# Optimization experiments

Measured on AMD Instinct MI355X. Metric: run time of the kernel, lower is better.

## Reference

```python
import jax, jax.numpy as jnp
import numpy as np

N = 50000
E = 400000
IN_C = 512
HID = 64
OUT_C = 40
H = 4
NEG_SLOPE = 0.2
EPS = 1e-16  # PyG softmax denominator epsilon


def glorot(key, shape, fan_in, fan_out):
    limit = float(np.sqrt(6.0 / (fan_in + fan_out)))
    return jax.random.uniform(key, shape, jnp.float32, -limit, limit)


def setup_inputs() -> dict:
    key = jax.random.key(0)
    ks = jax.random.split(key, 8)
    x = jax.random.normal(ks[0], (N, IN_C), jnp.float32)
    # random edges guaranteed to have src != dst (forward adds exactly one self-loop per node)
    src = jax.random.randint(ks[1], (E,), 0, N)
    off = jax.random.randint(ks[2], (E,), 1, N)
    dst = (src + off) % N
    edge_index = jnp.stack([src, dst], axis=0).astype(jnp.int64)
    W1 = glorot(ks[3], (IN_C, H * HID), IN_C, H * HID)
    b1 = jnp.zeros((H * HID,), jnp.float32)
    W2 = glorot(ks[4], (H * HID, H * OUT_C), H * HID, H * OUT_C)
    b2 = jnp.zeros((OUT_C,), jnp.float32)
    return {"x": x, "edge_index": edge_index, "W1": W1, "b1": b1, "W2": W2, "b2": b2}


def _supergat_layer(x, src, dst, W, b, heads, out_c, concat):
    n = x.shape[0]
    h = (x @ W).reshape(n, heads, out_c)            # [N,H,C]
    x_i = h[dst]                                    # [E',H,C] target
    x_j = h[src]                                    # [E',H,C] source
    # MX attention with return_logits=True inside message(): plain dot-product logits
    alpha = jnp.sum(x_i * x_j, axis=-1)             # [E',H]
    alpha = jax.nn.leaky_relu(alpha, NEG_SLOPE)
    # segment softmax over destination node
    amax = jax.ops.segment_max(alpha, dst, num_segments=n)
    alpha = jnp.exp(alpha - amax[dst])
    denom = jax.ops.segment_sum(alpha, dst, num_segments=n)
    alpha = alpha / (denom[dst] + EPS)
    out = jax.ops.segment_sum(x_j * alpha[:, :, None], dst, num_segments=n)  # [N,H,C]
    if concat:
        out = out.reshape(n, heads * out_c)
    else:
        out = out.mean(axis=1)
    return out + b


def reference(x, edge_index, W1, b1, W2, b2):
    # add_self_loops (input edges contain no self loops by construction)
    loop = jnp.arange(N, dtype=edge_index.dtype)
    src = jnp.concatenate([edge_index[0], loop])
    dst = jnp.concatenate([edge_index[1], loop])
    h = _supergat_layer(x, src, dst, W1, b1, H, HID, concat=True)
    h = jax.nn.elu(h)
    out = _supergat_layer(h, src, dst, W2, b2, H, OUT_C, concat=False)
    logp = jax.nn.log_softmax(out, axis=-1)
    att_loss = jnp.zeros((1,), jnp.float32)  # eval mode: get_attention_loss returns 0
    return logp, att_loss
```

## Files before the change

### kernel.cpp

```cpp
#include <hip/hip_runtime.h>
#include <cstddef>
#include <cstdint>

#define HEADS 4
#define OUTC  40
#define NEG   0.2f
#define EPSV  1e-16f

typedef __bf16 bf16x8 __attribute__((ext_vector_type(8)));
typedef float  floatx4 __attribute__((ext_vector_type(4)));

__device__ __forceinline__ void split_bf16(float a, unsigned& hi, unsigned& lo) {
  unsigned u = __float_as_uint(a);
  hi = u >> 16;
  float hf = __uint_as_float(u & 0xFFFF0000u);
  lo = __float_as_uint(a - hf) >> 16;
}

__device__ __forceinline__ void dma16(const void* g, void* l) {
  __builtin_amdgcn_global_load_lds(
      (const __attribute__((address_space(1))) unsigned int*)g,
      (__attribute__((address_space(3))) unsigned int*)l, 16, 0, 0);
}

__global__ void hist_k(const int* __restrict__ dst, int* __restrict__ cnt, int E) {
  int e = blockIdx.x * blockDim.x + threadIdx.x;
  if (e < E) atomicAdd(&cnt[dst[e]], 1);
}

__global__ __launch_bounds__(1024) void scanA_k(const int* __restrict__ cnt,
                                                int* __restrict__ rp,
                                                int* __restrict__ bsum, int n) {
  __shared__ int sh[1024];
  int i = blockIdx.x * 1024 + threadIdx.x;
  int v = (i < n) ? cnt[i] : 0;
  sh[threadIdx.x] = v;
  __syncthreads();
  for (int d = 1; d < 1024; d <<= 1) {
    int t = (threadIdx.x >= d) ? sh[threadIdx.x - d] : 0;
    __syncthreads();
    sh[threadIdx.x] += t;
    __syncthreads();
  }
  if (i < n) rp[i] = sh[threadIdx.x] - v;
  if (threadIdx.x == 1023) bsum[blockIdx.x] = sh[1023];
}

__global__ void scanC_k(int* __restrict__ rp, const int* __restrict__ bsum,
                        int n, int nb) {
  int i = blockIdx.x * blockDim.x + threadIdx.x;
  if (i < n) {
    int b = i >> 10;
    int off = 0;
    for (int j = 0; j < b; ++j) off += bsum[j];
    rp[i] += off;
  }
  if (i == 0) {
    int tot = 0;
    for (int j = 0; j < nb; ++j) tot += bsum[j];
    rp[n] = tot;
  }
}

__global__ void scatter_k(const int* __restrict__ src, const int* __restrict__ dst,
                          const int* __restrict__ rp, int* __restrict__ cur,
                          int* __restrict__ out, int E) {
  int e = blockIdx.x * blockDim.x + threadIdx.x;
  if (e < E) {
    int d = dst[e];
    int p = rp[d] + atomicAdd(&cur[d], 1);
    out[p] = src[e];
  }
}

__global__ void convW_k(const float* __restrict__ W1, unsigned short* __restrict__ Wh1,
                        unsigned short* __restrict__ Wl1,
                        const float* __restrict__ W2, unsigned short* __restrict__ Wh2,
                        unsigned short* __restrict__ Wl2) {
  int id = blockIdx.x * 256 + threadIdx.x;
  if (id < 256 * 512) {
    int n = id >> 9, k = id & 511;
    unsigned h, l;
    split_bf16(W1[k * 256 + n], h, l);
    Wh1[id] = (unsigned short)h;
    Wl1[id] = (unsigned short)l;
  } else {
    int id2 = id - 256 * 512;
    int n = id2 >> 8, k = id2 & 255;
    int hh = n >> 6, c = n & 63;
    float a = (c < OUTC) ? W2[k * 160 + hh * OUTC + c] : 0.f;
    unsigned h, l;
    split_bf16(a, h, l);
    Wh2[id2] = (unsigned short)h;
    Wl2[id2] = (unsigned short)l;
  }
}

template <bool A_FP32, bool COMPACT>
__global__ __launch_bounds__(256) void gemm_dma(const void* Aptr_h, const void* Aptr_l,
                                                const unsigned short* __restrict__ Bh,
                                                const unsigned short* __restrict__ Bl,
                                                float* __restrict__ C, int M, int K) {
  __shared__ __align__(16) unsigned char lds[65536];
  const int tid = threadIdx.x;
  const int lane = tid & 63;
  const int w = tid >> 6;
  const int wr = w >> 1, wc = w & 1;
  const int row0 = blockIdx.y * 128;
  const int col0 = blockIdx.x * 128;
  const int fr = lane & 15, fq = lane >> 4;
  const int swz8 = fr & 7;
  const int swz4 = (fr & 3) ^ ((fr >> 2) & 1);
  const int srcA8 = (lane & 7) ^ (lane >> 3);
  const int srcB4 = (lane & 3) ^ ((lane >> 2) & 3) ^ ((lane >> 4) & 1);

  floatx4 acc[4][4];
#pragma unroll
  for (int i = 0; i < 4; ++i)
#pragma unroll
    for (int j = 0; j < 4; ++j) acc[i][j] = (floatx4){0.f, 0.f, 0.f, 0.f};

  const float* Af32 = (const float*)Aptr_h;
  const unsigned short* Agh = (const unsigned short*)Aptr_h;
  const unsigned short* Agl = (const unsigned short*)Aptr_l;

#define DMA_TILE(K0, BASE)                                                          \
  do {                                                                              \
    if (A_FP32) {                                                                   \
      _Pragma("unroll") for (int t = 0; t < 4; ++t) {                               \
        int arow = w * 32 + t * 8 + (lane >> 3);                                    \
        int gr = row0 + arow; gr = gr < M ? gr : M - 1;                             \
        dma16(&Af32[(size_t)gr * K + (K0) + srcA8 * 4],                             \
              lds + (BASE) + (size_t)(w * 32 + t * 8) * 128);                       \
      }                                                                             \
    } else {                                                                        \
      _Pragma("unroll") for (int t = 0; t < 2; ++t) {                               \
        int arow = w * 32 + t * 16 + (lane >> 2);                                   \
        int gr = row0 + arow; gr = gr < M ? gr : M - 1;                             \
        size_t go = (size_t)gr * K + (K0) + srcB4 * 8;                              \
        dma16(&Agh[go], lds + (BASE) + (size_t)(w * 32 + t * 16) * 64);             \
        dma16(&Agl[go], lds + (BASE) + 8192 + (size_t)(w * 32 + t * 16) * 64);      \
      }                                                                             \
    }                                                                               \
    _Pragma("unroll") for (int t = 0; t < 2; ++t) {                                 \
      int nrow = w * 32 + t * 16 + (lane >> 2);                                     \
      size_t go = (size_t)(col0 + nrow) * K + (K0) + srcB4 * 8;                     \
      dma16(&Bh[go], lds + (BASE) + 16384 + (size_t)(w * 32 + t * 16) * 64);        \
      dma16(&Bl[go], lds + (BASE) + 24576 + (size_t)(w * 32 + t * 16) * 64);        \
    }                                                                               \
  } while (0)

  const int nk = K >> 5;
  DMA_TILE(0, 0);
  for (int k = 0; k < nk; ++k) {
    const int cur = (k & 1) << 15;
    if (k + 1 < nk) {
      DMA_TILE((k + 1) << 5, ((k + 1) & 1) << 15);
      asm volatile("s_waitcnt vmcnt(8)" ::: "memory");
    } else {
      asm volatile("s_waitcnt vmcnt(0)" ::: "memory");
    }
    asm volatile("s_barrier" ::: "memory");

    bf16x8 ah[4], al[4], bh[4], bl[4];
#pragma unroll
    for (int i = 0; i < 4; ++i) {
      int arow = wr * 64 + i * 16 + fr;
      if (A_FP32) {
        const unsigned char* pa = lds + cur + (size_t)arow * 128;
        float4 v0 = *(const float4*)(pa + (((fq * 2) ^ swz8) * 16));
        float4 v1 = *(const float4*)(pa + (((fq * 2 + 1) ^ swz8) * 16));
        unsigned u0 = __float_as_uint(v0.x), u1 = __float_as_uint(v0.y);
        unsigned u2 = __float_as_uint(v0.z), u3 = __float_as_uint(v0.w);
        unsigned u4 = __float_as_uint(v1.x), u5 = __float_as_uint(v1.y);
        unsigned u6 = __float_as_uint(v1.z), u7 = __float_as_uint(v1.w);
        uint4 H;
        H.x = (u0 >> 16) | (u1 & 0xFFFF0000u);
        H.y = (u2 >> 16) | (u3 & 0xFFFF0000u);
        H.z = (u4 >> 16) | (u5 & 0xFFFF0000u);
        H.w = (u6 >> 16) | (u7 & 0xFFFF0000u);
        uint4 L;
        L.x = (__float_as_uint(v0.x - __uint_as_float(u0 & 0xFFFF0000u)) >> 16) |
              (__float_as_uint(v0.y - __uint_as_float(u1 & 0xFFFF0000u)) & 0xFFFF0000u);
        L.y = (__float_as_uint(v0.z - __uint_as_float(u2 & 0xFFFF0000u)) >> 16) |
              (__float_as_uint(v0.w - __uint_as_float(u3 & 0xFFFF0000u)) & 0xFFFF0000u);
        L.z = (__float_as_uint(v1.x - __uint_as_float(u4 & 0xFFFF0000u)) >> 16) |
              (__float_as_uint(v1.y - __uint_as_float(u5 & 0xFFFF0000u)) & 0xFFFF0000u);
        L.w = (__float_as_uint(v1.z - __uint_as_float(u6 & 0xFFFF0000u)) >> 16) |
              (__float_as_uint(v1.w - __uint_as_float(u7 & 0xFFFF0000u)) & 0xFFFF0000u);
        ah[i] = *(bf16x8*)&H;
        al[i] = *(bf16x8*)&L;
      } else {
        ah[i] = *(bf16x8*)(lds + cur + (size_t)arow * 64 + ((fq ^ swz4) * 16));
        al[i] = *(bf16x8*)(lds + cur + 8192 + (size_t)arow * 64 + ((fq ^ swz4) * 16));
      }
      int brow = wc * 64 + i * 16 + fr;
      bh[i] = *(bf16x8*)(lds + cur + 16384 + (size_t)brow * 64 + ((fq ^ swz4) * 16));
      bl[i] = *(bf16x8*)(lds + cur + 24576 + (size_t)brow * 64 + ((fq ^ swz4) * 16));
    }
#pragma unroll
    for (int i = 0; i < 4; ++i)
#pragma unroll
      for (int j = 0; j < 4; ++j) {
        acc[i][j] = __builtin_amdgcn_mfma_f32_16x16x32_bf16(ah[i], bh[j], acc[i][j], 0, 0, 0);
        acc[i][j] = __builtin_amdgcn_mfma_f32_16x16x32_bf16(ah[i], bl[j], acc[i][j], 0, 0, 0);
        acc[i][j] = __builtin_amdgcn_mfma_f32_16x16x32_bf16(al[i], bh[j], acc[i][j], 0, 0, 0);
      }
    asm volatile("s_barrier" ::: "memory");
  }
#undef DMA_TILE

#pragma unroll
  for (int i = 0; i < 4; ++i) {
    int grow_base = row0 + wr * 64 + i * 16 + fq * 4;
#pragma unroll
    for (int r = 0; r < 4; ++r) {
      int grow = grow_base + r;
      if (grow < M) {
        if (COMPACT) {
          int head = blockIdx.x * 2 + wc;
#pragma unroll
          for (int j = 0; j < 4; ++j) {
            int cc = j * 16 + fr;
            if (cc < OUTC) C[(size_t)grow * 160 + head * OUTC + cc] = acc[i][j][r];
          }
        } else {
#pragma unroll
          for (int j = 0; j < 4; ++j)
            C[(size_t)grow * 256 + col0 + wc * 64 + j * 16 + fr] = acc[i][j][r];
        }
      }
    }
  }
}

__global__ __launch_bounds__(256) void agg1_k(const float* __restrict__ h,
                                              const int* __restrict__ rp,
                                              const int* __restrict__ srt,
                                              const float* __restrict__ b1,
                                              unsigned short* __restrict__ outh,
                                              unsigned short* __restrict__ outl, int Nn) {
  int wv = threadIdx.x >> 6, lane = threadIdx.x & 63;
  int node = blockIdx.x * 4 + wv;
  if (node >= Nn) node = Nn - 1;
  const float4 xi = *(const float4*)&h[(size_t)node * 256 + lane * 4];
  float p = xi.x * xi.x + xi.y * xi.y + xi.z * xi.z + xi.w * xi.w;
  p += __shfl_xor(p, 1); p += __shfl_xor(p, 2); p += __shfl_xor(p, 4); p += __shfl_xor(p, 8);
  float a = p > 0.f ? p : NEG * p;
  float m = a, l = 1.f;
  float4 acc = xi;
  const int e0 = rp[node], e1 = rp[node + 1];
  int e = e0;
  for (; e + 2 <= e1; e += 2) {
    int s0 = srt[e], s1 = srt[e + 1];
    const float4 xj0 = *(const float4*)&h[(size_t)s0 * 256 + lane * 4];
    const float4 xj1 = *(const float4*)&h[(size_t)s1 * 256 + lane * 4];
    float q0 = xi.x * xj0.x + xi.y * xj0.y + xi.z * xj0.z + xi.w * xj0.w;
    float q1 = xi.x * xj1.x + xi.y * xj1.y + xi.z * xj1.z + xi.w * xj1.w;
    q0 += __shfl_xor(q0, 1); q1 += __shfl_xor(q1, 1);
    q0 += __shfl_xor(q0, 2); q1 += __shfl_xor(q1, 2);
    q0 += __shfl_xor(q0, 4); q1 += __shfl_xor(q1, 4);
    q0 += __shfl_xor(q0, 8); q1 += __shfl_xor(q1, 8);
    float a0 = q0 > 0.f ? q0 : NEG * q0;
    float a1 = q1 > 0.f ? q1 : NEG * q1;
    float nm = fmaxf(m, fmaxf(a0, a1));
    float sc = __expf(m - nm), w0 = __expf(a0 - nm), w1 = __expf(a1 - nm);
    l = l * sc + w0 + w1;
    acc.x = acc.x * sc + w0 * xj0.x + w1 * xj1.x;
    acc.y = acc.y * sc + w0 * xj0.y + w1 * xj1.y;
    acc.z = acc.z * sc + w0 * xj0.z + w1 * xj1.z;
    acc.w = acc.w * sc + w0 * xj0.w + w1 * xj1.w;
    m = nm;
  }
  if (e < e1) {
    int s = srt[e];
    const float4 xj = *(const float4*)&h[(size_t)s * 256 + lane * 4];
    float q = xi.x * xj.x + xi.y * xj.y + xi.z * xj.z + xi.w * xj.w;
    q += __shfl_xor(q, 1); q += __shfl_xor(q, 2); q += __shfl_xor(q, 4); q += __shfl_xor(q, 8);
    float al = q > 0.f ? q : NEG * q;
    float nm = fmaxf(m, al);
    float sc = __expf(m - nm), wt = __expf(al - nm);
    l = l * sc + wt;
    acc.x = acc.x * sc + wt * xj.x;
    acc.y = acc.y * sc + wt * xj.y;
    acc.z = acc.z * sc + wt * xj.z;
    acc.w = acc.w * sc + wt * xj.w;
    m = nm;
  }
  float inv = 1.f / (l + EPSV);
  const float4 bb = *(const float4*)&b1[lane * 4];
  float4 o;
  o.x = acc.x * inv + bb.x;
  o.y = acc.y * inv + bb.y;
  o.z = acc.z * inv + bb.z;
  o.w = acc.w * inv + bb.w;
  o.x = o.x > 0.f ? o.x : __expf(o.x) - 1.f;
  o.y = o.y > 0.f ? o.y : __expf(o.y) - 1.f;
  o.z = o.z > 0.f ? o.z : __expf(o.z) - 1.f;
  o.w = o.w > 0.f ? o.w : __expf(o.w) - 1.f;
  unsigned h0, l0, h1, l1, h2, l2, h3, l3;
  split_bf16(o.x, h0, l0);
  split_bf16(o.y, h1, l1);
  split_bf16(o.z, h2, l2);
  split_bf16(o.w, h3, l3);
  size_t base = (size_t)node * 256 + lane * 4;
  *(uint2*)&outh[base] = make_uint2(h0 | (h1 << 16), h2 | (h3 << 16));
  *(uint2*)&outl[base] = make_uint2(l0 | (l1 << 16), l2 | (l3 << 16));
}

__global__ __launch_bounds__(256) void agg2_k(const float* __restrict__ h,
                                              const int* __restrict__ rp,
                                              const int* __restrict__ srt,
                                              const float* __restrict__ b2,
                                              float* __restrict__ out, int Nn) {
  __shared__ float buf[4][160];
  int wv = threadIdx.x >> 6, lane = threadIdx.x & 63;
  int node = blockIdx.x * 4 + wv;
  if (node >= Nn) node = Nn - 1;
  const int head = lane >> 4, c4 = lane & 15;
  const bool act = c4 < 10;
  float4 xi = make_float4(0.f, 0.f, 0.f, 0.f);
  if (act) xi = *(const float4*)&h[(size_t)node * 160 + head * OUTC + c4 * 4];
  float p = xi.x * xi.x + xi.y * xi.y + xi.z * xi.z + xi.w * xi.w;
  p += __shfl_xor(p, 1); p += __shfl_xor(p, 2); p += __shfl_xor(p, 4); p += __shfl_xor(p, 8);
  float a = p > 0.f ? p : NEG * p;
  float m = a, l = 1.f;
  float4 acc = xi;
  const int e0 = rp[node], e1 = rp[node + 1];
  int e = e0;
  for (; e + 2 <= e1; e += 2) {
    int s0 = srt[e], s1 = srt[e + 1];
    float4 xj0 = make_float4(0.f, 0.f, 0.f, 0.f);
    float4 xj1 = make_float4(0.f, 0.f, 0.f, 0.f);
    if (act) {
      xj0 = *(const float4*)&h[(size_t)s0 * 160 + head * OUTC + c4 * 4];
      xj1 = *(const float4*)&h[(size_t)s1 * 160 + head * OUTC + c4 * 4];
    }
    float q0 = xi.x * xj0.x + xi.y * xj0.y + xi.z * xj0.z + xi.w * xj0.w;
    float q1 = xi.x * xj1.x + xi.y * xj1.y + xi.z * xj1.z + xi.w * xj1.w;
    q0 += __shfl_xor(q0, 1); q1 += __shfl_xor(q1, 1);
    q0 += __shfl_xor(q0, 2); q1 += __shfl_xor(q1, 2);
    q0 += __shfl_xor(q0, 4); q1 += __shfl_xor(q1, 4);
    q0 += __shfl_xor(q0, 8); q1 += __shfl_xor(q1, 8);
    float a0 = q0 > 0.f ? q0 : NEG * q0;
    float a1 = q1 > 0.f ? q1 : NEG * q1;
    float nm = fmaxf(m, fmaxf(a0, a1));
    float sc = __expf(m - nm), w0 = __expf(a0 - nm), w1 = __expf(a1 - nm);
    l = l * sc + w0 + w1;
    acc.x = acc.x * sc + w0 * xj0.x + w1 * xj1.x;
    acc.y = acc.y * sc + w0 * xj0.y + w1 * xj1.y;
    acc.z = acc.z * sc + w0 * xj0.z + w1 * xj1.z;
    acc.w = acc.w * sc + w0 * xj0.w + w1 * xj1.w;
    m = nm;
  }
  if (e < e1) {
    int s = srt[e];
    float4 xj = make_float4(0.f, 0.f, 0.f, 0.f);
    if (act) xj = *(const float4*)&h[(size_t)s * 160 + head * OUTC + c4 * 4];
    float q = xi.x * xj.x + xi.y * xj.y + xi.z * xj.z + xi.w * xj.w;
    q += __shfl_xor(q, 1); q += __shfl_xor(q, 2); q += __shfl_xor(q, 4); q += __shfl_xor(q, 8);
    float al = q > 0.f ? q : NEG * q;
    float nm = fmaxf(m, al);
    float sc = __expf(m - nm), wt = __expf(al - nm);
    l = l * sc + wt;
    acc.x = acc.x * sc + wt * xj.x;
    acc.y = acc.y * sc + wt * xj.y;
    acc.z = acc.z * sc + wt * xj.z;
    acc.w = acc.w * sc + wt * xj.w;
    m = nm;
  }
  float inv = 1.f / (l + EPSV);
  if (act) {
    float4 res;
    res.x = acc.x * inv; res.y = acc.y * inv; res.z = acc.z * inv; res.w = acc.w * inv;
    *(float4*)&buf[wv][head * OUTC + c4 * 4] = res;
  }
  __syncthreads();
  const bool valid = lane < OUTC;
  float v = 0.f;
  if (valid)
    v = 0.25f * (buf[wv][lane] + buf[wv][OUTC + lane] + buf[wv][2 * OUTC + lane] +
                 buf[wv][3 * OUTC + lane]) + b2[lane];
  float t = valid ? v : -1e30f;
#pragma unroll
  for (int off = 32; off; off >>= 1) t = fmaxf(t, __shfl_xor(t, off));
  float ex = valid ? __expf(v - t) : 0.f;
  float s = ex;
#pragma unroll
  for (int off = 32; off; off >>= 1) s += __shfl_xor(s, off);
  float lse = t + __logf(s);
  if (valid) out[(size_t)node * OUTC + lane] = v - lse;
  if (blockIdx.x == 0 && threadIdx.x == 0) out[(size_t)Nn * OUTC] = 0.f;
}

extern "C" void kernel_launch(void* const* d_in, const int* in_sizes, int n_in,
                              void* d_out, int out_size, void* d_ws, size_t ws_size,
                              hipStream_t stream) {
  const float* x  = (const float*)d_in[0];
  const int*   ei = (const int*)d_in[1];
  const float* W1 = (const float*)d_in[2];
  const float* b1 = (const float*)d_in[3];
  const float* W2 = (const float*)d_in[4];
  const float* b2 = (const float*)d_in[5];
  float* out = (float*)d_out;

  const int Nn = in_sizes[0] / 512;
  const int E  = in_sizes[1] / 2;
  const int* esrc = ei;
  const int* edst = ei + E;
  const int NB = (Nn + 1023) / 1024;

  char* ws = (char*)d_ws;
  const size_t szH = (size_t)Nn * 256 * sizeof(float);
  float* h1 = (float*)(ws);
  size_t off = szH;
  unsigned short* g1h = (unsigned short*)(ws + off); off += (size_t)Nn * 256 * 2;
  unsigned short* g1l = (unsigned short*)(ws + off); off += (size_t)Nn * 256 * 2;
  int* rp = (int*)(ws + off);   off += ((size_t)(Nn + 1) * 4 + 15) & ~(size_t)15;
  int* cnt = (int*)(ws + off);  off += ((size_t)Nn * 4 + 15) & ~(size_t)15;
  int* srt = (int*)(ws + off);  off += ((size_t)E * 4 + 15) & ~(size_t)15;
  int* bsum = (int*)(ws + off); off += 1024;
  unsigned short* Wh1 = (unsigned short*)(ws + off); off += (size_t)256 * 512 * 2;
  unsigned short* Wl1 = (unsigned short*)(ws + off); off += (size_t)256 * 512 * 2;
  unsigned short* Wh2 = (unsigned short*)(ws + off); off += (size_t)256 * 256 * 2;
  unsigned short* Wl2 = (unsigned short*)(ws + off); off += (size_t)256 * 256 * 2;
  float* h2 = h1;

  hipMemsetAsync(cnt, 0, (size_t)Nn * sizeof(int), stream);
  hist_k<<<(E + 255) / 256, 256, 0, stream>>>(edst, cnt, E);
  scanA_k<<<NB, 1024, 0, stream>>>(cnt, rp, bsum, Nn);
  scanC_k<<<(Nn + 255) / 256, 256, 0, stream>>>(rp, bsum, Nn, NB);
  hipMemsetAsync(cnt, 0, (size_t)Nn * sizeof(int), stream);
  scatter_k<<<(E + 255) / 256, 256, 0, stream>>>(esrc, edst, rp, cnt, srt, E);

  convW_k<<<768, 256, 0, stream>>>(W1, Wh1, Wl1, W2, Wh2, Wl2);

  gemm_dma<true, false>
      <<<dim3(2, (Nn + 127) / 128), 256, 0, stream>>>(x, nullptr, Wh1, Wl1, h1, Nn, 512);
  agg1_k<<<(Nn + 3) / 4, 256, 0, stream>>>(h1, rp, srt, b1, g1h, g1l, Nn);

  gemm_dma<false, true>
      <<<dim3(2, (Nn + 127) / 128), 256, 0, stream>>>(g1h, g1l, Wh2, Wl2, h2, Nn, 256);
  agg2_k<<<(Nn + 3) / 4, 256, 0, stream>>>(h2, rp, srt, b2, out, Nn);
}
```

Measured before the change: 399.3 us.

## Single-buffer A tile in GEMM for occupancy; unroll edge loops by four

The GEMM now double-buffers only the B tile and keeps a single A buffer, loading the next A tile after an extra barrier once all waves have read the current one. This shrinks LDS from 64KB to 48KB and adds a launch-bounds hint of three blocks, so more workgroups can be resident. In exchange it adds a second barrier per k-step and exposes A load latency. Both aggregation kernels also process four neighbor edges per iteration instead of two, so more gathers are in flight, with a loop handling leftover edges.

```diff
diff --git a/kernel.cpp b/kernel.cpp
--- a/kernel.cpp
+++ b/kernel.cpp
@@ -97,11 +97,11 @@
 }
 
 template <bool A_FP32, bool COMPACT>
-__global__ __launch_bounds__(256) void gemm_dma(const void* Aptr_h, const void* Aptr_l,
-                                                const unsigned short* __restrict__ Bh,
-                                                const unsigned short* __restrict__ Bl,
-                                                float* __restrict__ C, int M, int K) {
-  __shared__ __align__(16) unsigned char lds[65536];
+__global__ __launch_bounds__(256, 3) void gemm_dma(const void* Aptr_h, const void* Aptr_l,
+                                                   const unsigned short* __restrict__ Bh,
+                                                   const unsigned short* __restrict__ Bl,
+                                                   float* __restrict__ C, int M, int K) {
+  __shared__ __align__(16) unsigned char lds[49152];
   const int tid = threadIdx.x;
   const int lane = tid & 63;
   const int w = tid >> 6;
@@ -124,39 +124,45 @@
   const unsigned short* Agh = (const unsigned short*)Aptr_h;
   const unsigned short* Agl = (const unsigned short*)Aptr_l;
 
-#define DMA_TILE(K0, BASE)                                                          \
+#define DMA_A(K0)                                                                   \
   do {                                                                              \
     if (A_FP32) {                                                                   \
       _Pragma("unroll") for (int t = 0; t < 4; ++t) {                               \
         int arow = w * 32 + t * 8 + (lane >> 3);                                    \
         int gr = row0 + arow; gr = gr < M ? gr : M - 1;                             \
         dma16(&Af32[(size_t)gr * K + (K0) + srcA8 * 4],                             \
-              lds + (BASE) + (size_t)(w * 32 + t * 8) * 128);                       \
+              lds + (size_t)(w * 32 + t * 8) * 128);                                \
       }                                                                             \
     } else {                                                                        \
       _Pragma("unroll") for (int t = 0; t < 2; ++t) {                               \
         int arow = w * 32 + t * 16 + (lane >> 2);                                   \
         int gr = row0 + arow; gr = gr < M ? gr : M - 1;                             \
         size_t go = (size_t)gr * K + (K0) + srcB4 * 8;                              \
-        dma16(&Agh[go], lds + (BASE) + (size_t)(w * 32 + t * 16) * 64);             \
-        dma16(&Agl[go], lds + (BASE) + 8192 + (size_t)(w * 32 + t * 16) * 64);      \
+        dma16(&Agh[go], lds + (size_t)(w * 32 + t * 16) * 64);                      \
+        dma16(&Agl[go], lds + 8192 + (size_t)(w * 32 + t * 16) * 64);               \
       }                                                                             \
     }                                                                               \
+  } while (0)
+
+#define DMA_B(K0, BASE)                                                             \
+  do {                                                                              \
     _Pragma("unroll") for (int t = 0; t < 2; ++t) {                                 \
       int nrow = w * 32 + t * 16 + (lane >> 2);                                     \
       size_t go = (size_t)(col0 + nrow) * K + (K0) + srcB4 * 8;                     \
-      dma16(&Bh[go], lds + (BASE) + 16384 + (size_t)(w * 32 + t * 16) * 64);        \
-      dma16(&Bl[go], lds + (BASE) + 24576 + (size_t)(w * 32 + t * 16) * 64);        \
+      dma16(&Bh[go], lds + (BASE) + (size_t)(w * 32 + t * 16) * 64);                \
+      dma16(&Bl[go], lds + (BASE) + 8192 + (size_t)(w * 32 + t * 16) * 64);         \
     }                                                                               \
   } while (0)
 
   const int nk = K >> 5;
-  DMA_TILE(0, 0);
+  DMA_B(0, 16384);
+  DMA_A(0);
+  asm volatile("" ::: "memory");
   for (int k = 0; k < nk; ++k) {
-    const int cur = (k & 1) << 15;
+    const int bbase = 16384 + ((k & 1) << 14);
     if (k + 1 < nk) {
-      DMA_TILE((k + 1) << 5, ((k + 1) & 1) << 15);
-      asm volatile("s_waitcnt vmcnt(8)" ::: "memory");
+      DMA_B((k + 1) << 5, 16384 + (((k + 1) & 1) << 14));
+      asm volatile("s_waitcnt vmcnt(4)" ::: "memory");
     } else {
       asm volatile("s_waitcnt vmcnt(0)" ::: "memory");
     }
@@ -167,7 +173,7 @@
     for (int i = 0; i < 4; ++i) {
       int arow = wr * 64 + i * 16 + fr;
       if (A_FP32) {
-        const unsigned char* pa = lds + cur + (size_t)arow * 128;
+        const unsigned char* pa = lds + (size_t)arow * 128;
         float4 v0 = *(const float4*)(pa + (((fq * 2) ^ swz8) * 16));
         float4 v1 = *(const float4*)(pa + (((fq * 2 + 1) ^ swz8) * 16));
         unsigned u0 = __float_as_uint(v0.x), u1 = __float_as_uint(v0.y);
@@ -191,13 +197,17 @@
         ah[i] = *(bf16x8*)&H;
         al[i] = *(bf16x8*)&L;
       } else {
-        ah[i] = *(bf16x8*)(lds + cur + (size_t)arow * 64 + ((fq ^ swz4) * 16));
-        al[i] = *(bf16x8*)(lds + cur + 8192 + (size_t)arow * 64 + ((fq ^ swz4) * 16));
+        ah[i] = *(bf16x8*)(lds + (size_t)arow * 64 + ((fq ^ swz4) * 16));
+        al[i] = *(bf16x8*)(lds + 8192 + (size_t)arow * 64 + ((fq ^ swz4) * 16));
       }
       int brow = wc * 64 + i * 16 + fr;
-      bh[i] = *(bf16x8*)(lds + cur + 16384 + (size_t)brow * 64 + ((fq ^ swz4) * 16));
-      bl[i] = *(bf16x8*)(lds + cur + 24576 + (size_t)brow * 64 + ((fq ^ swz4) * 16));
+      bh[i] = *(bf16x8*)(lds + bbase + (size_t)brow * 64 + ((fq ^ swz4) * 16));
+      bl[i] = *(bf16x8*)(lds + bbase + 8192 + (size_t)brow * 64 + ((fq ^ swz4) * 16));
     }
+    asm volatile("s_waitcnt lgkmcnt(0)" ::: "memory");
+    asm volatile("s_barrier" ::: "memory");
+    if (k + 1 < nk) DMA_A((k + 1) << 5);
+
 #pragma unroll
     for (int i = 0; i < 4; ++i)
 #pragma unroll
@@ -206,9 +216,9 @@
         acc[i][j] = __builtin_amdgcn_mfma_f32_16x16x32_bf16(ah[i], bl[j], acc[i][j], 0, 0, 0);
         acc[i][j] = __builtin_amdgcn_mfma_f32_16x16x32_bf16(al[i], bh[j], acc[i][j], 0, 0, 0);
       }
-    asm volatile("s_barrier" ::: "memory");
-  }
-#undef DMA_TILE
+  }
+#undef DMA_A
+#undef DMA_B
 
 #pragma unroll
   for (int i = 0; i < 4; ++i) {
@@ -251,28 +261,36 @@
   float4 acc = xi;
   const int e0 = rp[node], e1 = rp[node + 1];
   int e = e0;
-  for (; e + 2 <= e1; e += 2) {
-    int s0 = srt[e], s1 = srt[e + 1];
+  for (; e + 4 <= e1; e += 4) {
+    int s0 = srt[e], s1 = srt[e + 1], s2 = srt[e + 2], s3 = srt[e + 3];
     const float4 xj0 = *(const float4*)&h[(size_t)s0 * 256 + lane * 4];
     const float4 xj1 = *(const float4*)&h[(size_t)s1 * 256 + lane * 4];
+    const float4 xj2 = *(const float4*)&h[(size_t)s2 * 256 + lane * 4];
+    const float4 xj3 = *(const float4*)&h[(size_t)s3 * 256 + lane * 4];
     float q0 = xi.x * xj0.x + xi.y * xj0.y + xi.z * xj0.z + xi.w * xj0.w;
     float q1 = xi.x * xj1.x + xi.y * xj1.y + xi.z * xj1.z + xi.w * xj1.w;
-    q0 += __shfl_xor(q0, 1); q1 += __shfl_xor(q1, 1);
-    q0 += __shfl_xor(q0, 2); q1 += __shfl_xor(q1, 2);
-    q0 += __shfl_xor(q0, 4); q1 += __shfl_xor(q1, 4);
-    q0 += __shfl_xor(q0, 8); q1 += __shfl_xor(q1, 8);
+    float q2 = xi.x * xj2.x + xi.y * xj2.y + xi.z * xj2.z + xi.w * xj2.w;
+    float q3 = xi.x * xj3.x + xi.y * xj3.y + xi.z * xj3.z + xi.w * xj3.w;
+    q0 += __shfl_xor(q0, 1); q1 += __shfl_xor(q1, 1); q2 += __shfl_xor(q2, 1); q3 += __shfl_xor(q3, 1);
+    q0 += __shfl_xor(q0, 2); q1 += __shfl_xor(q1, 2); q2 += __shfl_xor(q2, 2); q3 += __shfl_xor(q3, 2);
+    q0 += __shfl_xor(q0, 4); q1 += __shfl_xor(q1, 4); q2 += __shfl_xor(q2, 4); q3 += __shfl_xor(q3, 4);
+    q0 += __shfl_xor(q0, 8); q1 += __shfl_xor(q1, 8); q2 += __shfl_xor(q2, 8); q3 += __shfl_xor(q3, 8);
     float a0 = q0 > 0.f ? q0 : NEG * q0;
     float a1 = q1 > 0.f ? q1 : NEG * q1;
-    float nm = fmaxf(m, fmaxf(a0, a1));
-    float sc = __expf(m - nm), w0 = __expf(a0 - nm), w1 = __expf(a1 - nm);
-    l = l * sc + w0 + w1;
-    acc.x = acc.x * sc + w0 * xj0.x + w1 * xj1.x;
-    acc.y = acc.y * sc + w0 * xj0.y + w1 * xj1.y;
-    acc.z = acc.z * sc + w0 * xj0.z + w1 * xj1.z;
-    acc.w = acc.w * sc + w0 * xj0.w + w1 * xj1.w;
+    float a2 = q2 > 0.f ? q2 : NEG * q2;
+    float a3 = q3 > 0.f ? q3 : NEG * q3;
+    float nm = fmaxf(fmaxf(m, fmaxf(a0, a1)), fmaxf(a2, a3));
+    float sc = __expf(m - nm);
+    float w0 = __expf(a0 - nm), w1 = __expf(a1 - nm);
+    float w2 = __expf(a2 - nm), w3 = __expf(a3 - nm);
+    l = l * sc + w0 + w1 + w2 + w3;
+    acc.x = acc.x * sc + w0 * xj0.x + w1 * xj1.x + w2 * xj2.x + w3 * xj3.x;
+    acc.y = acc.y * sc + w0 * xj0.y + w1 * xj1.y + w2 * xj2.y + w3 * xj3.y;
+    acc.z = acc.z * sc + w0 * xj0.z + w1 * xj1.z + w2 * xj2.z + w3 * xj3.z;
+    acc.w = acc.w * sc + w0 * xj0.w + w1 * xj1.w + w2 * xj2.w + w3 * xj3.w;
     m = nm;
   }
-  if (e < e1) {
+  for (; e < e1; ++e) {
     int s = srt[e];
     const float4 xj = *(const float4*)&h[(size_t)s * 256 + lane * 4];
     float q = xi.x * xj.x + xi.y * xj.y + xi.z * xj.z + xi.w * xj.w;
@@ -328,32 +346,42 @@
   float4 acc = xi;
   const int e0 = rp[node], e1 = rp[node + 1];
   int e = e0;
-  for (; e + 2 <= e1; e += 2) {
-    int s0 = srt[e], s1 = srt[e + 1];
+  for (; e + 4 <= e1; e += 4) {
+    int s0 = srt[e], s1 = srt[e + 1], s2 = srt[e + 2], s3 = srt[e + 3];
     float4 xj0 = make_float4(0.f, 0.f, 0.f, 0.f);
     float4 xj1 = make_float4(0.f, 0.f, 0.f, 0.f);
+    float4 xj2 = make_float4(0.f, 0.f, 0.f, 0.f);
+    float4 xj3 = make_float4(0.f, 0.f, 0.f, 0.f);
     if (act) {
       xj0 = *(const float4*)&h[(size_t)s0 * 160 + head * OUTC + c4 * 4];
       xj1 = *(const float4*)&h[(size_t)s1 * 160 + head * OUTC + c4 * 4];
+      xj2 = *(const float4*)&h[(size_t)s2 * 160 + head * OUTC + c4 * 4];
+      xj3 = *(const float4*)&h[(size_t)s3 * 160 + head * OUTC + c4 * 4];
     }
     float q0 = xi.x * xj0.x + xi.y * xj0.y + xi.z * xj0.z + xi.w * xj0.w;
     float q1 = xi.x * xj1.x + xi.y * xj1.y + xi.z * xj1.z + xi.w * xj1.w;
-    q0 += __shfl_xor(q0, 1); q1 += __shfl_xor(q1, 1);
-    q0 += __shfl_xor(q0, 2); q1 += __shfl_xor(q1, 2);
-    q0 += __shfl_xor(q0, 4); q1 += __shfl_xor(q1, 4);
-    q0 += __shfl_xor(q0, 8); q1 += __shfl_xor(q1, 8);
+    float q2 = xi.x * xj2.x + xi.y * xj2.y + xi.z * xj2.z + xi.w * xj2.w;
+    float q3 = xi.x * xj3.x + xi.y * xj3.y + xi.z * xj3.z + xi.w * xj3.w;
+    q0 += __shfl_xor(q0, 1); q1 += __shfl_xor(q1, 1); q2 += __shfl_xor(q2, 1); q3 += __shfl_xor(q3, 1);
+    q0 += __shfl_xor(q0, 2); q1 += __shfl_xor(q1, 2); q2 += __shfl_xor(q2, 2); q3 += __shfl_xor(q3, 2);
+    q0 += __shfl_xor(q0, 4); q1 += __shfl_xor(q1, 4); q2 += __shfl_xor(q2, 4); q3 += __shfl_xor(q3, 4);
+    q0 += __shfl_xor(q0, 8); q1 += __shfl_xor(q1, 8); q2 += __shfl_xor(q2, 8); q3 += __shfl_xor(q3, 8);
     float a0 = q0 > 0.f ? q0 : NEG * q0;
     float a1 = q1 > 0.f ? q1 : NEG * q1;
-    float nm = fmaxf(m, fmaxf(a0, a1));
-    float sc = __expf(m - nm), w0 = __expf(a0 - nm), w1 = __expf(a1 - nm);
-    l = l * sc + w0 + w1;
-    acc.x = acc.x * sc + w0 * xj0.x + w1 * xj1.x;
-    acc.y = acc.y * sc + w0 * xj0.y + w1 * xj1.y;
-    acc.z = acc.z * sc + w0 * xj0.z + w1 * xj1.z;
-    acc.w = acc.w * sc + w0 * xj0.w + w1 * xj1.w;
+    float a2 = q2 > 0.f ? q2 : NEG * q2;
+    float a3 = q3 > 0.f ? q3 : NEG * q3;
+    float nm = fmaxf(fmaxf(m, fmaxf(a0, a1)), fmaxf(a2, a3));
+    float sc = __expf(m - nm);
+    float w0 = __expf(a0 - nm), w1 = __expf(a1 - nm);
+    float w2 = __expf(a2 - nm), w3 = __expf(a3 - nm);
+    l = l * sc + w0 + w1 + w2 + w3;
+    acc.x = acc.x * sc + w0 * xj0.x + w1 * xj1.x + w2 * xj2.x + w3 * xj3.x;
+    acc.y = acc.y * sc + w0 * xj0.y + w1 * xj1.y + w2 * xj2.y + w3 * xj3.y;
+    acc.z = acc.z * sc + w0 * xj0.z + w1 * xj1.z + w2 * xj2.z + w3 * xj3.z;
+    acc.w = acc.w * sc + w0 * xj0.w + w1 * xj1.w + w2 * xj2.w + w3 * xj3.w;
     m = nm;
   }
-  if (e < e1) {
+  for (; e < e1; ++e) {
     int s = srt[e];
     float4 xj = make_float4(0.f, 0.f, 0.f, 0.f);
     if (act) xj = *(const float4*)&h[(size_t)s * 160 + head * OUTC + c4 * 4];
```

Measured after the change: 394.0 us. Within noise of the previous version (-1.3%).
